# Optimization experiments

Hardware: AMD Instinct MI355X
Metric: run time of the kernel (lower is better)

Reference implementation:

```python
import jax, jax.numpy as jnp
import numpy as np

B, T, INP_DIM, H = 32, 2000, 4, 512
TC = 0.01  # t_const


def setup_inputs() -> dict:
    key = jax.random.key(0)
    ks = jax.random.split(key, 10)
    inp = jax.random.normal(ks[0], (B, T, INP_DIM), dtype=jnp.float32)
    hn = jax.random.uniform(ks[1], (1, B, 2 * H), dtype=jnp.float32)
    x = jnp.zeros((1, B, 2 * H), jnp.float32)
    inhib_stim = jnp.zeros((B, T, 2 * H), jnp.float32)
    u = lambda k, s, hi: jax.random.uniform(k, s, jnp.float32, 0.0, hi)
    str2str_w = u(ks[2], (H, H), 0.01)
    alm2alm_w = u(ks[3], (H, H), 0.01)
    alm2str_w = u(ks[4], (H, H), 0.01)
    str2alm_w = u(ks[5], (H, H), 0.01)
    inp_weight = u(ks[6], (INP_DIM, 2 * H), 0.01)
    sparse_mask = (jax.random.uniform(ks[7], (H, H)) < 0.1).astype(jnp.float32)
    str2str_fixed = u(ks[8], (H, H), 0.001) * sparse_mask
    str2str_mask = jnp.zeros((H, H), jnp.float32)
    n_inhib = int(0.3 * H)
    alm2str_mask = jnp.concatenate(
        [jnp.ones((H, H - n_inhib), jnp.float32), jnp.zeros((H, n_inhib), jnp.float32)], axis=1)
    alm2alm_sign = jnp.concatenate(
        [jnp.ones((H - n_inhib,), jnp.float32), -jnp.ones((n_inhib,), jnp.float32)])
    str_d1_mask = jnp.concatenate([jnp.ones((H,), jnp.float32), jnp.zeros((H,), jnp.float32)])
    return dict(inp=inp, hn=hn, x=x, inhib_stim=inhib_stim,
                str2str_w=str2str_w, alm2alm_w=alm2alm_w, alm2str_w=alm2str_w,
                str2alm_w=str2alm_w, inp_weight=inp_weight,
                str2str_fixed=str2str_fixed, str2str_mask=str2str_mask,
                alm2str_mask=alm2str_mask, alm2alm_sign=alm2alm_sign,
                str_d1_mask=str_d1_mask)


def _build_wrec(str2str_w, alm2alm_w, alm2str_w, str2alm_w,
                str2str_fixed, str2str_mask, alm2str_mask, alm2alm_sign):
    clip01 = lambda w: jnp.clip(w, 1e-15, 1.0)  # F.hardtanh(w, 1e-15, 1)
    str2str = -(str2str_mask * clip01(str2str_w) + str2str_fixed)      # @ (-I)
    alm2alm = clip01(alm2alm_w) * alm2alm_sign[None, :]                # @ diag(sign)
    alm2str = alm2str_mask * clip01(alm2str_w)
    str2alm = clip01(str2alm_w)
    W_str = jnp.concatenate([str2str, alm2str], axis=1)
    W_alm = jnp.concatenate([str2alm, alm2alm], axis=1)
    return jnp.concatenate([W_str, W_alm], axis=0)  # [2H, 2H]


def reference(inp, hn, x, inhib_stim, str2str_w, alm2alm_w, alm2str_w, str2alm_w,
              inp_weight, str2str_fixed, str2str_mask, alm2str_mask,
              alm2alm_sign, str_d1_mask):
    W_rec = _build_wrec(str2str_w, alm2alm_w, alm2str_w, str2alm_w,
                        str2str_fixed, str2str_mask, alm2str_mask, alm2alm_sign)
    # input drive precomputed for all steps: [B, T, 2H] (noise=False path)
    drive = jnp.einsum('bti,ih->bth', inp, inp_weight) * str_d1_mask + inhib_stim
    h0 = hn[0]  # [B, 2H]

    def step(h, d_t):
        h_new = jax.nn.relu(h + TC * (-h + h @ W_rec.T + d_t))
        return h_new, h_new

    _, hs = jax.lax.scan(step, h0, jnp.swapaxes(drive, 0, 1))  # [T, B, 2H]
    rnn_out = jnp.swapaxes(hs, 0, 1)                            # [B, T, 2H]
    x_out = jnp.broadcast_to(x[0][:, None, :], rnn_out.shape)   # x never updated
    hn_last = rnn_out[:, -1, :][None]
    x_last = x_out[:, -1, :][None]
    return (hn_last, rnn_out, x_last, x_out)
```

## Files before the change

kernel.cpp:

```cpp
#include <hip/hip_runtime.h>
#include <stdint.h>

#define H2      1024
#define TSTEPS  2000
#define TC_C    0.01f

#define NGROUPS   8
#define WG_PER_G  8
#define BPG       4
#define ROWS_WG   128
#define NTHR      512
#define NBLOCKS   (NGROUPS * WG_PER_G)

#define OFF_RNN   32768
#define OFF_XL    (32768 + 65536000)
#define OFF_XO    (OFF_XL + 32768)


typedef __attribute__((ext_vector_type(8))) short bf16x8;
typedef __attribute__((ext_vector_type(4))) float f32x4;

__device__ __forceinline__ float clip01(float w) {
  return fminf(fmaxf(w, 1e-15f), 1.0f);
}
__device__ __forceinline__ uint32_t f2bf(float x) {
  uint32_t u = __float_as_uint(x);
  return ((u + 0x7fffu + ((u >> 16) & 1u)) >> 16) & 0xffffu;
}

__global__ void stralm_init_kernel(const float* __restrict__ hn,
                                   const float* __restrict__ x,
                                   float* __restrict__ out,
                                   float* __restrict__ ws) {
  const int tid = blockIdx.x * 256 + threadIdx.x;
  const int b  = tid >> 11;
  const int r  = tid & 2047;
  const int jq = (r & 255) * 4;
  const int t0 = (r >> 8) * 250;
  const float4 xv = *(const float4*)(x + b * H2 + jq);
  float* xo = out + OFF_XO;
  for (int i = 0; i < 250; ++i) {
    const int t = t0 + i;
    *(float4*)(xo + (size_t)(b * TSTEPS + t) * H2 + jq) = xv;
  }
  if (tid < 8192) {
    const float4 hv = *(const float4*)(hn + tid * 4);
    uint32_t* bufu = (uint32_t*)ws;
    uint2 pk;
    pk.x = f2bf(hv.x) | (f2bf(hv.y) << 16);
    pk.y = f2bf(hv.z) | (f2bf(hv.w) << 16);
    *(uint2*)(bufu + tid * 2) = pk;
    *(float4*)(out + OFF_XL + tid * 4) = *(const float4*)(x + tid * 4);
  }
  if (tid < 256) ((int*)ws)[32768 + tid] = 0;
}

__global__ __launch_bounds__(NTHR, 2) void stralm_rnn_kernel(
    const float* __restrict__ inp,
    const float* __restrict__ hn,
    const float* __restrict__ inhib,
    const float* __restrict__ ss_w, const float* __restrict__ a2a_w,
    const float* __restrict__ a2s_w, const float* __restrict__ s2a_w,
    const float* __restrict__ iw,
    const float* __restrict__ ss_fix, const float* __restrict__ ss_mask,
    const float* __restrict__ a2s_mask, const float* __restrict__ sign_v,
    const float* __restrict__ d1mask,
    float* __restrict__ out, float* __restrict__ ws) {
  __shared__ __align__(16) float smem[8448];

  const int tid = threadIdx.x;
  const int g   = blockIdx.x & 7;
  const int wg  = blockIdx.x >> 3;
  const int r0  = wg * ROWS_WG;
  const int l   = tid & 63;
  const int wv  = tid >> 6;

  uint32_t* bufu  = (uint32_t*)ws;
  int*      flags = (int*)ws + 32768 + g * 32;

  bf16x8 afr[8][4];
  {
    unsigned short* wstage = (unsigned short*)smem;
#pragma unroll
    for (int mt = 0; mt < 8; ++mt) {
      __syncthreads();
      for (int i = 0; i < 32; ++i) {
        const int idx = i * NTHR + tid;
        const int jt  = idx >> 10;
        const int k   = idx & 1023;
        const int jg  = r0 + mt * 16 + jt;
        const int jq  = jg & 511;
        float w;
        if (jg < 512) {
          if (k < 512)
            w = -(ss_mask[jq * 512 + k] * clip01(ss_w[jq * 512 + k]) +
                  ss_fix[jq * 512 + k]);
          else {
            const int kk = k - 512;
            w = a2s_mask[jq * 512 + kk] * clip01(a2s_w[jq * 512 + kk]);
          }
        } else {
          if (k < 512)
            w = clip01(s2a_w[jq * 512 + k]);
          else {
            const int kk = k - 512;
            w = clip01(a2a_w[jq * 512 + kk]) * sign_v[kk];
          }
        }
        wstage[jt * 1032 + k] = (unsigned short)f2bf(w);
      }
      __syncthreads();
#pragma unroll
      for (int kt = 0; kt < 4; ++kt)
        afr[mt][kt] = *(const bf16x8*)&wstage[(l & 15) * 1032 + wv * 128 +
                                              kt * 32 + (l >> 4) * 8];
    }
  }
  __syncthreads();

  uint32_t* h_lds = (uint32_t*)smem;
  float*    red   = smem + 2080;

  const bool eth  = (tid < 256);
  const int  sb   = tid >> 6;
  const int  ml   = (tid & 63) * 2;
  const int  bg   = g * BPG + sb;
  const int  grow = r0 + ml;
  float2 iwv[4]; float2 dmv = {0.f, 0.f};
  float2 inh_cur = {0.f, 0.f};
  float4 ip_cur  = {0.f, 0.f, 0.f, 0.f};
  float  hold0 = 0.f, hold1 = 0.f;
  if (eth) {
#pragma unroll
    for (int i = 0; i < 4; ++i) iwv[i] = *(const float2*)(iw + i * H2 + grow);
    dmv     = *(const float2*)(d1mask + grow);
    inh_cur = *(const float2*)(inhib + (size_t)bg * TSTEPS * H2 + grow);
    ip_cur  = *(const float4*)(inp + bg * (TSTEPS * 4));
    const float2 h0 = *(const float2*)(hn + bg * H2 + grow);
    hold0 = h0.x; hold1 = h0.y;
  }

  for (int t = 0; t < TSTEPS; ++t) {
    const int p = t & 1;
    if (tid < WG_PER_G) {
      const int* fl = flags + tid;
      while (__hip_atomic_load(fl, __ATOMIC_RELAXED,
                               __HIP_MEMORY_SCOPE_AGENT) < t)
        __builtin_amdgcn_s_sleep(1);
    }
    __syncthreads();

    uint32_t hv[4];
    const int ubase = p * 16384 + g * 2048;
#pragma unroll
    for (int j = 0; j < 4; ++j)
      hv[j] = __hip_atomic_load(bufu + ubase + j * NTHR + tid,
                                __ATOMIC_RELAXED, __HIP_MEMORY_SCOPE_AGENT);
#pragma unroll
    for (int j = 0; j < 4; ++j) {
      const int f = j * NTHR + tid;
      h_lds[(f >> 9) * 516 + (f & 511)] = hv[j];
    }
    __syncthreads();

    const int bb = l & 3;
    const int kb = (l >> 4) * 8;
    const unsigned short* hs = (const unsigned short*)h_lds;
    bf16x8 bfr[4];
#pragma unroll
    for (int kt = 0; kt < 4; ++kt)
      bfr[kt] = *(const bf16x8*)&hs[bb * 1032 + wv * 128 + kt * 32 + kb];

    f32x4 acc[8];
#pragma unroll
    for (int mt = 0; mt < 8; ++mt) acc[mt] = (f32x4){0.f, 0.f, 0.f, 0.f};
#pragma unroll
    for (int mt = 0; mt < 8; ++mt)
#pragma unroll
      for (int kt = 0; kt < 4; ++kt)
        acc[mt] = __builtin_amdgcn_mfma_f32_16x16x32_bf16(afr[mt][kt], bfr[kt],
                                                          acc[mt], 0, 0, 0);
    if ((l & 15) < 4) {
      const int n = l & 15, h4 = l >> 4;
#pragma unroll
      for (int mt = 0; mt < 8; ++mt)
#pragma unroll
        for (int q = 0; q < 4; ++q)
          red[wv * 536 + n * 134 + mt * 16 + h4 * 4 + q] = acc[mt][q];
    }
    __syncthreads();

    if (eth) {
      float s0 = 0.f, s1 = 0.f;
#pragma unroll
      for (int w8 = 0; w8 < 8; ++w8) {
        const float2 rv = *(const float2*)&red[w8 * 536 + sb * 134 + ml];
        s0 += rv.x; s1 += rv.y;
      }
      const float din0 = dmv.x * (iwv[0].x * ip_cur.x + iwv[1].x * ip_cur.y +
                                  iwv[2].x * ip_cur.z + iwv[3].x * ip_cur.w) +
                         inh_cur.x;
      const float din1 = dmv.y * (iwv[0].y * ip_cur.x + iwv[1].y * ip_cur.y +
                                  iwv[2].y * ip_cur.z + iwv[3].y * ip_cur.w) +
                         inh_cur.y;
      const float hn0 = fmaxf(0.f, (1.f - TC_C) * hold0 + TC_C * (s0 + din0));
      const float hn1 = fmaxf(0.f, (1.f - TC_C) * hold1 + TC_C * (s1 + din1));
      hold0 = hn0; hold1 = hn1;
      const uint32_t pk = f2bf(hn0) | (f2bf(hn1) << 16);
      __hip_atomic_store(bufu + (p ^ 1) * 16384 + bg * 512 + (grow >> 1), pk,
                         __ATOMIC_RELAXED, __HIP_MEMORY_SCOPE_AGENT);
      const uint64_t u64 = (uint64_t)__float_as_uint(hn0) |
                           ((uint64_t)__float_as_uint(hn1) << 32);
      __builtin_nontemporal_store(
          u64, (uint64_t*)(out + OFF_RNN +
                           (size_t)bg * (TSTEPS * H2) + (size_t)t * H2 + grow));
      if (t == TSTEPS - 1) {
        out[bg * H2 + grow]     = hn0;
        out[bg * H2 + grow + 1] = hn1;
      }
    }
    asm volatile("s_waitcnt vmcnt(0)" ::: "memory");
    __syncthreads();
    if (tid == 0)
      __hip_atomic_store(flags + wg, t + 1, __ATOMIC_RELAXED,
                         __HIP_MEMORY_SCOPE_AGENT);
    if (eth) {
      const int tn = (t < TSTEPS - 1) ? t + 1 : TSTEPS - 1;
      inh_cur = *(const float2*)(inhib + ((size_t)bg * TSTEPS + tn) * H2 + grow);
      ip_cur  = *(const float4*)(inp + bg * (TSTEPS * 4) + tn * 4);
    }
  }
}

extern "C" void kernel_launch(void* const* d_in, const int* in_sizes, int n_in,
                              void* d_out, int out_size, void* d_ws,
                              size_t ws_size, hipStream_t stream) {
  const float* inp      = (const float*)d_in[0];
  const float* hn       = (const float*)d_in[1];
  const float* x        = (const float*)d_in[2];
  const float* inhib    = (const float*)d_in[3];
  const float* ss_w     = (const float*)d_in[4];
  const float* a2a_w    = (const float*)d_in[5];
  const float* a2s_w    = (const float*)d_in[6];
  const float* s2a_w    = (const float*)d_in[7];
  const float* iw       = (const float*)d_in[8];
  const float* ss_fix   = (const float*)d_in[9];
  const float* ss_mask  = (const float*)d_in[10];
  const float* a2s_mask = (const float*)d_in[11];
  const float* sign_v   = (const float*)d_in[12];
  const float* d1mask   = (const float*)d_in[13];
  float* out = (float*)d_out;
  float* ws  = (float*)d_ws;

  hipLaunchKernelGGL(stralm_init_kernel, dim3(256), dim3(256), 0, stream,
                     hn, x, out, ws);
  hipLaunchKernelGGL(stralm_rnn_kernel, dim3(NBLOCKS), dim3(NTHR), 0, stream,
                     inp, hn, inhib, ss_w, a2a_w, a2s_w, s2a_w, iw, ss_fix,
                     ss_mask, a2s_mask, sign_v, d1mask, out, ws);
}
```

Baseline: 4.858 ms.

## Replace flag barrier with per-element step-tagged h exchange and per-wave full-K MFMA

New measurement: 6.875 ms. 41.5% more time.

```diff
diff --git a/kernel.cpp b/kernel.cpp
--- a/kernel.cpp
+++ b/kernel.cpp
@@ -43,19 +43,17 @@
     const int t = t0 + i;
     *(float4*)(xo + (size_t)(b * TSTEPS + t) * H2 + jq) = xv;
   }
-  if (tid < 8192) {
-    const float4 hv = *(const float4*)(hn + tid * 4);
-    uint32_t* bufu = (uint32_t*)ws;
-    uint2 pk;
-    pk.x = f2bf(hv.x) | (f2bf(hv.y) << 16);
-    pk.y = f2bf(hv.z) | (f2bf(hv.w) << 16);
-    *(uint2*)(bufu + tid * 2) = pk;
+  uint64_t* buf64 = (uint64_t*)ws;
+  if (tid < 16384) {
+    const float2 hv = *(const float2*)(hn + tid * 2);
+    buf64[tid]         = (uint64_t)(f2bf(hv.x) | (f2bf(hv.y) << 16));
+    buf64[16384 + tid] = 0xFFFFFFFF00000000ULL;
+  }
+  if (tid < 8192)
     *(float4*)(out + OFF_XL + tid * 4) = *(const float4*)(x + tid * 4);
-  }
-  if (tid < 256) ((int*)ws)[32768 + tid] = 0;
-}
-
-__global__ __launch_bounds__(NTHR, 2) void stralm_rnn_kernel(
+}
+
+__global__ __launch_bounds__(NTHR, 1) void stralm_rnn_kernel(
     const float* __restrict__ inp,
     const float* __restrict__ hn,
     const float* __restrict__ inhib,
@@ -66,7 +64,7 @@
     const float* __restrict__ a2s_mask, const float* __restrict__ sign_v,
     const float* __restrict__ d1mask,
     float* __restrict__ out, float* __restrict__ ws) {
-  __shared__ __align__(16) float smem[8448];
+  __shared__ __align__(16) uint32_t smem[8256];
 
   const int tid = threadIdx.x;
   const int g   = blockIdx.x & 7;
@@ -75,13 +73,11 @@
   const int l   = tid & 63;
   const int wv  = tid >> 6;
 
-  uint32_t* bufu  = (uint32_t*)ws;
-  int*      flags = (int*)ws + 32768 + g * 32;
-
-  bf16x8 afr[8][4];
+  uint64_t* buf64 = (uint64_t*)ws;
+
+  bf16x8 afr[32];
   {
     unsigned short* wstage = (unsigned short*)smem;
-#pragma unroll
     for (int mt = 0; mt < 8; ++mt) {
       __syncthreads();
       for (int i = 0; i < 32; ++i) {
@@ -110,123 +106,90 @@
         wstage[jt * 1032 + k] = (unsigned short)f2bf(w);
       }
       __syncthreads();
+      if (wv == mt) {
 #pragma unroll
-      for (int kt = 0; kt < 4; ++kt)
-        afr[mt][kt] = *(const bf16x8*)&wstage[(l & 15) * 1032 + wv * 128 +
-                                              kt * 32 + (l >> 4) * 8];
+        for (int kt = 0; kt < 32; ++kt)
+          afr[kt] = *(const bf16x8*)&wstage[(l & 15) * 1032 + kt * 32 +
+                                            (l >> 4) * 8];
+      }
     }
   }
   __syncthreads();
 
-  uint32_t* h_lds = (uint32_t*)smem;
-  float*    red   = smem + 2080;
-
-  const bool eth  = (tid < 256);
-  const int  sb   = tid >> 6;
-  const int  ml   = (tid & 63) * 2;
-  const int  bg   = g * BPG + sb;
-  const int  grow = r0 + ml;
-  float2 iwv[4]; float2 dmv = {0.f, 0.f};
-  float2 inh_cur = {0.f, 0.f};
-  float4 ip_cur  = {0.f, 0.f, 0.f, 0.f};
-  float  hold0 = 0.f, hold1 = 0.f;
-  if (eth) {
-#pragma unroll
-    for (int i = 0; i < 4; ++i) iwv[i] = *(const float2*)(iw + i * H2 + grow);
-    dmv     = *(const float2*)(d1mask + grow);
-    inh_cur = *(const float2*)(inhib + (size_t)bg * TSTEPS * H2 + grow);
+  uint32_t* h_lds = smem;
+
+  const int  n    = l & 15;
+  const bool act  = (n < 4);
+  const int  bg   = g * BPG + (act ? n : 0);
+  const int  grow = r0 + wv * 16 + (l >> 4) * 4;
+  float4 iwr0 = {}, iwr1 = {}, iwr2 = {}, iwr3 = {}, dmr = {}, hold = {};
+  float4 inh_cur = {}, ip_cur = {};
+  if (act) {
+    iwr0 = *(const float4*)(iw + 0 * H2 + grow);
+    iwr1 = *(const float4*)(iw + 1 * H2 + grow);
+    iwr2 = *(const float4*)(iw + 2 * H2 + grow);
+    iwr3 = *(const float4*)(iw + 3 * H2 + grow);
+    dmr  = *(const float4*)(d1mask + grow);
+    hold = *(const float4*)(hn + bg * H2 + grow);
+    inh_cur = *(const float4*)(inhib + (size_t)bg * TSTEPS * H2 + grow);
     ip_cur  = *(const float4*)(inp + bg * (TSTEPS * 4));
-    const float2 h0 = *(const float2*)(hn + bg * H2 + grow);
-    hold0 = h0.x; hold1 = h0.y;
-  }
+  }
+  const int bb = l & 3;
 
   for (int t = 0; t < TSTEPS; ++t) {
     const int p = t & 1;
-    if (tid < WG_PER_G) {
-      const int* fl = flags + tid;
-      while (__hip_atomic_load(fl, __ATOMIC_RELAXED,
-                               __HIP_MEMORY_SCOPE_AGENT) < t)
-        __builtin_amdgcn_s_sleep(1);
-    }
-    __syncthreads();
-
-    uint32_t hv[4];
-    const int ubase = p * 16384 + g * 2048;
-#pragma unroll
-    for (int j = 0; j < 4; ++j)
-      hv[j] = __hip_atomic_load(bufu + ubase + j * NTHR + tid,
-                                __ATOMIC_RELAXED, __HIP_MEMORY_SCOPE_AGENT);
+    const uint64_t* src = buf64 + p * 16384 + g * 2048 + tid;
+    uint32_t* dst = h_lds + p * 2064 + tid;
 #pragma unroll
     for (int j = 0; j < 4; ++j) {
-      const int f = j * NTHR + tid;
-      h_lds[(f >> 9) * 516 + (f & 511)] = hv[j];
+      uint64_t v = __hip_atomic_load(src + j * 512, __ATOMIC_RELAXED,
+                                     __HIP_MEMORY_SCOPE_AGENT);
+      while ((int)(v >> 32) < t) {
+        __builtin_amdgcn_s_sleep(1);
+        v = __hip_atomic_load(src + j * 512, __ATOMIC_RELAXED,
+                              __HIP_MEMORY_SCOPE_AGENT);
+      }
+      dst[j * 516] = (uint32_t)v;
     }
     __syncthreads();
 
-    const int bb = l & 3;
-    const int kb = (l >> 4) * 8;
-    const unsigned short* hs = (const unsigned short*)h_lds;
-    bf16x8 bfr[4];
+    const unsigned short* hs =
+        (const unsigned short*)h_lds + p * 4128 + bb * 1032 + (l >> 4) * 8;
+    f32x4 acc = {0.f, 0.f, 0.f, 0.f};
 #pragma unroll
-    for (int kt = 0; kt < 4; ++kt)
-      bfr[kt] = *(const bf16x8*)&hs[bb * 1032 + wv * 128 + kt * 32 + kb];
-
-    f32x4 acc[8];
-#pragma unroll
-    for (int mt = 0; mt < 8; ++mt) acc[mt] = (f32x4){0.f, 0.f, 0.f, 0.f};
-#pragma unroll
-    for (int mt = 0; mt < 8; ++mt)
-#pragma unroll
-      for (int kt = 0; kt < 4; ++kt)
-        acc[mt] = __builtin_amdgcn_mfma_f32_16x16x32_bf16(afr[mt][kt], bfr[kt],
-                                                          acc[mt], 0, 0, 0);
-    if ((l & 15) < 4) {
-      const int n = l & 15, h4 = l >> 4;
-#pragma unroll
-      for (int mt = 0; mt < 8; ++mt)
-#pragma unroll
-        for (int q = 0; q < 4; ++q)
-          red[wv * 536 + n * 134 + mt * 16 + h4 * 4 + q] = acc[mt][q];
-    }
-    __syncthreads();
-
-    if (eth) {
-      float s0 = 0.f, s1 = 0.f;
-#pragma unroll
-      for (int w8 = 0; w8 < 8; ++w8) {
-        const float2 rv = *(const float2*)&red[w8 * 536 + sb * 134 + ml];
-        s0 += rv.x; s1 += rv.y;
-      }
-      const float din0 = dmv.x * (iwv[0].x * ip_cur.x + iwv[1].x * ip_cur.y +
-                                  iwv[2].x * ip_cur.z + iwv[3].x * ip_cur.w) +
-                         inh_cur.x;
-      const float din1 = dmv.y * (iwv[0].y * ip_cur.x + iwv[1].y * ip_cur.y +
-                                  iwv[2].y * ip_cur.z + iwv[3].y * ip_cur.w) +
-                         inh_cur.y;
-      const float hn0 = fmaxf(0.f, (1.f - TC_C) * hold0 + TC_C * (s0 + din0));
-      const float hn1 = fmaxf(0.f, (1.f - TC_C) * hold1 + TC_C * (s1 + din1));
-      hold0 = hn0; hold1 = hn1;
-      const uint32_t pk = f2bf(hn0) | (f2bf(hn1) << 16);
-      __hip_atomic_store(bufu + (p ^ 1) * 16384 + bg * 512 + (grow >> 1), pk,
+    for (int kt = 0; kt < 32; ++kt) {
+      const bf16x8 bfr = *(const bf16x8*)&hs[kt * 32];
+      acc = __builtin_amdgcn_mfma_f32_16x16x32_bf16(afr[kt], bfr, acc, 0, 0, 0);
+    }
+
+    if (act) {
+      const float d0 = dmr.x * (iwr0.x * ip_cur.x + iwr1.x * ip_cur.y +
+                                iwr2.x * ip_cur.z + iwr3.x * ip_cur.w) + inh_cur.x;
+      const float d1 = dmr.y * (iwr0.y * ip_cur.x + iwr1.y * ip_cur.y +
+                                iwr2.y * ip_cur.z + iwr3.y * ip_cur.w) + inh_cur.y;
+      const float d2 = dmr.z * (iwr0.z * ip_cur.x + iwr1.z * ip_cur.y +
+                                iwr2.z * ip_cur.z + iwr3.z * ip_cur.w) + inh_cur.z;
+      const float d3 = dmr.w * (iwr0.w * ip_cur.x + iwr1.w * ip_cur.y +
+                                iwr2.w * ip_cur.z + iwr3.w * ip_cur.w) + inh_cur.w;
+      const float h0 = fmaxf(0.f, (1.f - TC_C) * hold.x + TC_C * (acc[0] + d0));
+      const float h1 = fmaxf(0.f, (1.f - TC_C) * hold.y + TC_C * (acc[1] + d1));
+      const float h2 = fmaxf(0.f, (1.f - TC_C) * hold.z + TC_C * (acc[2] + d2));
+      const float h3 = fmaxf(0.f, (1.f - TC_C) * hold.w + TC_C * (acc[3] + d3));
+      hold = (float4){h0, h1, h2, h3};
+      const uint64_t tagv = ((uint64_t)(uint32_t)(t + 1)) << 32;
+      uint64_t* ep = buf64 + (p ^ 1) * 16384 + bg * 512 + (grow >> 1);
+      __hip_atomic_store(ep, tagv | (uint64_t)(f2bf(h0) | (f2bf(h1) << 16)),
                          __ATOMIC_RELAXED, __HIP_MEMORY_SCOPE_AGENT);
-      const uint64_t u64 = (uint64_t)__float_as_uint(hn0) |
-                           ((uint64_t)__float_as_uint(hn1) << 32);
+      __hip_atomic_store(ep + 1, tagv | (uint64_t)(f2bf(h2) | (f2bf(h3) << 16)),
+                         __ATOMIC_RELAXED, __HIP_MEMORY_SCOPE_AGENT);
+      const f32x4 hv4 = {h0, h1, h2, h3};
       __builtin_nontemporal_store(
-          u64, (uint64_t*)(out + OFF_RNN +
-                           (size_t)bg * (TSTEPS * H2) + (size_t)t * H2 + grow));
-      if (t == TSTEPS - 1) {
-        out[bg * H2 + grow]     = hn0;
-        out[bg * H2 + grow + 1] = hn1;
-      }
-    }
-    asm volatile("s_waitcnt vmcnt(0)" ::: "memory");
-    __syncthreads();
-    if (tid == 0)
-      __hip_atomic_store(flags + wg, t + 1, __ATOMIC_RELAXED,
-                         __HIP_MEMORY_SCOPE_AGENT);
-    if (eth) {
+          hv4, (f32x4*)(out + OFF_RNN + (size_t)bg * (TSTEPS * H2) +
+                        (size_t)t * H2 + grow));
+      if (t == TSTEPS - 1)
+        *(float4*)(out + bg * H2 + grow) = (float4){h0, h1, h2, h3};
       const int tn = (t < TSTEPS - 1) ? t + 1 : TSTEPS - 1;
-      inh_cur = *(const float2*)(inhib + ((size_t)bg * TSTEPS + tn) * H2 + grow);
+      inh_cur = *(const float4*)(inhib + ((size_t)bg * TSTEPS + tn) * H2 + grow);
       ip_cur  = *(const float4*)(inp + bg * (TSTEPS * 4) + tn * 4);
     }
   }
```
